# Kernel tuning notes

Hardware: AMD Instinct MI355X
Metric: run time of the kernel (lower is better)

## Reference

```python
import jax, jax.numpy as jnp
import numpy as np

N_NODES = 100000
N_EDGES = 1600000
F_IN, HID, N_CLS = 128, 128, 40


def setup_inputs() -> dict:
    key = jax.random.key(0)
    k1, k2, k3, k4 = jax.random.split(key, 4)
    x = jax.random.normal(k1, (N_NODES, F_IN), dtype=jnp.float32)
    edge_index = jax.random.randint(k2, (2, N_EDGES), 0, N_NODES, dtype=jnp.int64)
    # Glorot-style init for the two GCNConv linear layers
    W1 = jax.random.normal(k3, (F_IN, HID), dtype=jnp.float32) / np.sqrt(F_IN)
    b1 = jnp.zeros((HID,), dtype=jnp.float32)
    W2 = jax.random.normal(k4, (HID, N_CLS), dtype=jnp.float32) / np.sqrt(HID)
    b2 = jnp.zeros((N_CLS,), dtype=jnp.float32)
    return {"x": x, "edge_index": edge_index, "W1": W1, "b1": b1, "W2": W2, "b2": b2}


def gcn_conv(x, src, dst, W, b, n_nodes):
    # x' = D^{-1/2} (A + I) D^{-1/2} X W + b  (PyG GCNConv with default gcn_norm)
    h = x @ W  # [N, out]
    deg = jax.ops.segment_sum(jnp.ones_like(dst, h.dtype), dst, num_segments=n_nodes)
    dinv = jax.lax.rsqrt(deg)  # deg >= 1 because self-loops are included
    norm = dinv[src] * dinv[dst]  # [E']
    msg = h[src] * norm[:, None]  # gather + scale (irregular, memory-bound)
    out = jax.ops.segment_sum(msg, dst, num_segments=n_nodes)  # scatter-add
    return out + b


def reference(x, edge_index, W1, b1, W2, b2):
    n = x.shape[0]
    loops = jnp.arange(n, dtype=edge_index.dtype)
    src = jnp.concatenate([edge_index[0], loops])  # add self-loops once
    dst = jnp.concatenate([edge_index[1], loops])
    h = jax.nn.relu(gcn_conv(x, src, dst, W1, b1, n))
    # dropout is identity in eval mode
    logits = gcn_conv(h, src, dst, W2, b2, n)
    return jax.nn.log_softmax(logits, axis=1)
```

## Files before the change

kernel.cpp:

```cpp
#include <hip/hip_runtime.h>
#include <cstdint>
#include <cmath>

#define F_INN 128
#define HIDD  128
#define NCLS  40

#define BUCK_SHIFT 7
#define BUCK_NODES 128
#define MAXBUCK 1024
#define NSPLIT 8
#define CHUNK 8192

typedef unsigned int u32;
typedef unsigned short u16;
typedef __attribute__((ext_vector_type(8))) short bf16x8;
typedef __attribute__((ext_vector_type(4))) float f32x4;

static __device__ __forceinline__ float bflo(u32 u) { return __builtin_bit_cast(float, u << 16); }
static __device__ __forceinline__ float bfhi(u32 u) { return __builtin_bit_cast(float, u & 0xffff0000u); }
static __device__ __forceinline__ u16 f2bf(float f) {
    u32 u = __builtin_bit_cast(u32, f);
    return (u16)((u + 0x7fffu + ((u >> 16) & 1u)) >> 16);
}
static __device__ __forceinline__ u32 pack2(float a, float b) {
    return (u32)f2bf(a) | ((u32)f2bf(b) << 16);
}


__global__ __launch_bounds__(256) void k_s1(const int* __restrict__ ei, u32* __restrict__ gtot,
                                            int E, int nbuck) {
    __shared__ u32 cnt[MAXBUCK];
    int t = threadIdx.x;
    for (int i = t; i < nbuck; i += 256) cnt[i] = 0;
    __syncthreads();
    int x = blockIdx.x & (NSPLIT - 1);
    int e0 = blockIdx.x * CHUNK;
    int n = min(CHUNK, E - e0);
    const int* dst = ei + E;
    for (int i = t; i < n; i += 256)
        atomicAdd(&cnt[dst[e0 + i] >> BUCK_SHIFT], 1u);
    __syncthreads();
    for (int b = t; b < nbuck; b += 256) {
        u32 c = cnt[b];
        if (c) atomicAdd(&gtot[(b << 3) | x], c);
    }
}


__global__ __launch_bounds__(256) void k_s2(const u32* __restrict__ gtot, u32* __restrict__ base,
                                            u32* __restrict__ cursor, int m) {
    __shared__ u32 part[256];
    int t = threadIdx.x;
    u32 local[32];
    u32 s = 0;
#pragma unroll
    for (int j = 0; j < 32; ++j) {
        int i = t * 32 + j;
        u32 v = (i < m) ? gtot[i] : 0u;
        local[j] = s;
        s += v;
    }
    part[t] = s;
    __syncthreads();
    for (int off = 1; off < 256; off <<= 1) {
        u32 v = (t >= off) ? part[t - off] : 0u;
        __syncthreads();
        part[t] += v;
        __syncthreads();
    }
    u32 pre = (t == 0) ? 0u : part[t - 1];
#pragma unroll
    for (int j = 0; j < 32; ++j) {
        int i = t * 32 + j;
        if (i < m) { u32 bb = pre + local[j]; base[i] = bb; cursor[i] = bb; }
    }
    if (t == 255) base[m] = part[255];
}


__global__ __launch_bounds__(256) void k_s3(const int* __restrict__ ei, u32* __restrict__ cursor,
                                            u32* __restrict__ arr, int E, int nbuck) {
    __shared__ u32 cnt[MAXBUCK];
    __shared__ u32 lbase[MAXBUCK];
    int t = threadIdx.x;
    for (int i = t; i < nbuck; i += 256) cnt[i] = 0;
    __syncthreads();
    int x = blockIdx.x & (NSPLIT - 1);
    int e0 = blockIdx.x * CHUNK;
    int n = min(CHUNK, E - e0);
    const int* src = ei;
    const int* dst = ei + E;
    for (int i = t; i < n; i += 256)
        atomicAdd(&cnt[dst[e0 + i] >> BUCK_SHIFT], 1u);
    __syncthreads();
    for (int b = t; b < nbuck; b += 256) {
        u32 c = cnt[b];
        lbase[b] = c ? atomicAdd(&cursor[(b << 3) | x], c) : 0u;
    }
    __syncthreads();
    for (int i = t; i < nbuck; i += 256) cnt[i] = 0;
    __syncthreads();
    for (int i = t; i < n; i += 256) {
        int s = src[e0 + i], d = dst[e0 + i];
        int b = d >> BUCK_SHIFT;
        u32 off = atomicAdd(&cnt[b], 1u);
        arr[lbase[b] + off] = ((u32)s << BUCK_SHIFT) | (u32)(d & (BUCK_NODES - 1));
    }
}


__global__ __launch_bounds__(256) void k_sortb(const u32* __restrict__ arr, const u32* __restrict__ base,
                                               int* __restrict__ csr, int* __restrict__ rowptr,
                                               float* __restrict__ dinv, int N, int nbuck) {
    __shared__ u32 cnt[BUCK_NODES];
    __shared__ u32 ex[BUCK_NODES];
    __shared__ u32 cur[BUCK_NODES];
    int b = blockIdx.x, t = threadIdx.x;
    int node0 = b << BUCK_SHIFT;
    if (t < BUCK_NODES) cnt[t] = 0;
    __syncthreads();
    u32 s0 = base[b << 3], s1 = base[(b + 1) << 3];
    for (u32 i = s0 + t; i < s1; i += 256)
        atomicAdd(&cnt[arr[i] & (u32)(BUCK_NODES - 1)], 1u);
    __syncthreads();
    if (t < BUCK_NODES) ex[t] = cnt[t];
    __syncthreads();
    for (int off = 1; off < BUCK_NODES; off <<= 1) {
        u32 v = 0;
        if (t < BUCK_NODES && t >= off) v = ex[t - off];
        __syncthreads();
        if (t < BUCK_NODES) ex[t] += v;
        __syncthreads();
    }
    if (t < BUCK_NODES) {
        int node = node0 + t;
        u32 excl = ex[t] - cnt[t];
        cur[t] = s0 + excl;
        if (node <= N) rowptr[node] = (int)(s0 + excl);
        if (node < N) dinv[node] = rsqrtf((float)(cnt[t] + 1));
    }
    if (t == 0 && b == nbuck - 1) rowptr[N] = (int)s1;
    __syncthreads();
    for (u32 i = s0 + t; i < s1; i += 256) {
        u32 pk = arr[i];
        int d = (int)(pk & (u32)(BUCK_NODES - 1));
        u32 pos = atomicAdd(&cur[d], 1u);
        csr[pos] = (int)(pk >> BUCK_SHIFT);
    }
}


__global__ __launch_bounds__(256) void k_gemm1m(const float* __restrict__ X, const float* __restrict__ W,
                                                u32* __restrict__ H, int M) {
    __shared__ u32 xa[128 * 64];
    __shared__ u32 wb[128 * 64];
    int tid = threadIdx.x;
    int row0 = blockIdx.x * 128;
    for (int j = tid; j < 64 * 128; j += 256) {
        int n = j & 127, kp = j >> 7;
        u32 v = pack2(W[(2 * kp) * 128 + n], W[(2 * kp + 1) * 128 + n]);
        wb[n * 64 + (kp ^ ((n & 7) << 2))] = v;
    }
    for (int j = tid; j < 128 * 64; j += 256) {
        int r = j >> 6, c = j & 63;
        int gr = row0 + r;
        u32 v = 0;
        if (gr < M) {
            float2 xv = *(const float2*)&X[(size_t)gr * 128 + 2 * c];
            v = pack2(xv.x, xv.y);
        }
        xa[r * 64 + (c ^ ((r & 7) << 2))] = v;
    }
    __syncthreads();
    int lane = tid & 63, wv = tid >> 6;
    int rw = wv * 32;
    int lr = lane & 15, lg = lane >> 4;
    f32x4 acc[2][8] = {};
    for (int kk = 0; kk < 4; ++kk) {
        int c0 = kk * 16 + lg * 4;
        int ra0 = rw + lr, ra1 = rw + 16 + lr;
        bf16x8 a0 = *(const bf16x8*)&xa[ra0 * 64 + (c0 ^ ((ra0 & 7) << 2))];
        bf16x8 a1 = *(const bf16x8*)&xa[ra1 * 64 + (c0 ^ ((ra1 & 7) << 2))];
#pragma unroll
        for (int nf = 0; nf < 8; ++nf) {
            int bn = nf * 16 + lr;
            bf16x8 bfr = *(const bf16x8*)&wb[bn * 64 + (c0 ^ ((bn & 7) << 2))];
            acc[0][nf] = __builtin_amdgcn_mfma_f32_16x16x32_bf16(a0, bfr, acc[0][nf], 0, 0, 0);
            acc[1][nf] = __builtin_amdgcn_mfma_f32_16x16x32_bf16(a1, bfr, acc[1][nf], 0, 0, 0);
        }
    }
    u16* Hs = (u16*)H;
#pragma unroll
    for (int rf = 0; rf < 2; ++rf) {
#pragma unroll
        for (int nf = 0; nf < 8; ++nf) {
            int col = nf * 16 + lr;
#pragma unroll
            for (int j = 0; j < 4; ++j) {
                int gr = row0 + rw + rf * 16 + lg * 4 + j;
                if (gr < M) Hs[(size_t)gr * 128 + col] = f2bf(acc[rf][nf][j]);
            }
        }
    }
}


__global__ __launch_bounds__(256) void k_gemm2m(const u32* __restrict__ A, const float* __restrict__ W,
                                                u32* __restrict__ H, int M) {
    __shared__ u32 xa[128 * 64];
    __shared__ u32 wb[48 * 64];
    int tid = threadIdx.x;
    int row0 = blockIdx.x * 128;
    for (int j = tid; j < 64 * 64; j += 256) {
        int n = j & 63, kp = j >> 6;
        if (n < 48) {
            u32 v = 0;
            if (n < 40) v = pack2(W[(2 * kp) * 40 + n], W[(2 * kp + 1) * 40 + n]);
            wb[n * 64 + (kp ^ ((n & 7) << 2))] = v;
        }
    }
    for (int j = tid; j < 128 * 64; j += 256) {
        int r = j >> 6, c = j & 63;
        int gr = row0 + r;
        u32 v = (gr < M) ? A[(size_t)gr * 64 + c] : 0u;
        xa[r * 64 + (c ^ ((r & 7) << 2))] = v;
    }
    __syncthreads();
    int lane = tid & 63, wv = tid >> 6;
    int rw = wv * 32;
    int lr = lane & 15, lg = lane >> 4;
    f32x4 acc[2][3] = {};
    for (int kk = 0; kk < 4; ++kk) {
        int c0 = kk * 16 + lg * 4;
        int ra0 = rw + lr, ra1 = rw + 16 + lr;
        bf16x8 a0 = *(const bf16x8*)&xa[ra0 * 64 + (c0 ^ ((ra0 & 7) << 2))];
        bf16x8 a1 = *(const bf16x8*)&xa[ra1 * 64 + (c0 ^ ((ra1 & 7) << 2))];
#pragma unroll
        for (int nf = 0; nf < 3; ++nf) {
            int bn = nf * 16 + lr;
            bf16x8 bfr = *(const bf16x8*)&wb[bn * 64 + (c0 ^ ((bn & 7) << 2))];
            acc[0][nf] = __builtin_amdgcn_mfma_f32_16x16x32_bf16(a0, bfr, acc[0][nf], 0, 0, 0);
            acc[1][nf] = __builtin_amdgcn_mfma_f32_16x16x32_bf16(a1, bfr, acc[1][nf], 0, 0, 0);
        }
    }
    u16* Hs = (u16*)H;
#pragma unroll
    for (int rf = 0; rf < 2; ++rf) {
#pragma unroll
        for (int nf = 0; nf < 3; ++nf) {
            int col = nf * 16 + lr;
            if (col < 40) {
#pragma unroll
                for (int j = 0; j < 4; ++j) {
                    int gr = row0 + rw + rf * 16 + lg * 4 + j;
                    if (gr < M) Hs[(size_t)gr * 64 + col] = f2bf(acc[rf][nf][j]);
                }
            }
        }
    }
}


__global__ __launch_bounds__(256) void k_agg1(const u32* __restrict__ H1, const int* __restrict__ csr,
                                              const int* __restrict__ rowptr, const float* __restrict__ dinv,
                                              const float* __restrict__ b1, u32* __restrict__ A1, int n) {
    int node = (int)((blockIdx.x * 256 + threadIdx.x) >> 6);
    int lane = threadIdx.x & 63;
    if (node >= n) return;
    float di = dinv[node];
    u32 us = H1[(size_t)node * 64 + lane];
    float wself = di * di;
    float ax = wself * bflo(us), ay = wself * bfhi(us);
    int e0 = rowptr[node], e1 = rowptr[node + 1];
    int e = e0;
    for (; e + 3 < e1; e += 4) {
        int s0 = csr[e], s1 = csr[e + 1], s2 = csr[e + 2], s3 = csr[e + 3];
        float w0 = dinv[s0] * di, w1 = dinv[s1] * di, w2 = dinv[s2] * di, w3 = dinv[s3] * di;
        u32 u0 = H1[(size_t)s0 * 64 + lane];
        u32 u1 = H1[(size_t)s1 * 64 + lane];
        u32 u2 = H1[(size_t)s2 * 64 + lane];
        u32 u3 = H1[(size_t)s3 * 64 + lane];
        ax += w0 * bflo(u0) + w1 * bflo(u1) + w2 * bflo(u2) + w3 * bflo(u3);
        ay += w0 * bfhi(u0) + w1 * bfhi(u1) + w2 * bfhi(u2) + w3 * bfhi(u3);
    }
    for (; e < e1; ++e) {
        int s0 = csr[e];
        float w0 = dinv[s0] * di;
        u32 u0 = H1[(size_t)s0 * 64 + lane];
        ax += w0 * bflo(u0);
        ay += w0 * bfhi(u0);
    }
    ax = fmaxf(ax + b1[lane * 2], 0.f);
    ay = fmaxf(ay + b1[lane * 2 + 1], 0.f);
    A1[(size_t)node * 64 + lane] = pack2(ax, ay);
}


__global__ __launch_bounds__(256) void k_agg2(const u32* __restrict__ H2, const int* __restrict__ csr,
                                              const int* __restrict__ rowptr, const float* __restrict__ dinv,
                                              const float* __restrict__ b2, float* __restrict__ out, int n) {
    int wid = (int)((blockIdx.x * 256 + threadIdx.x) >> 6);
    int lane = threadIdx.x & 63;
    int half = lane >> 5, l = lane & 31;
    int node = wid * 2 + half;
    int nc = (node < n) ? node : (n - 1);
    bool wr = (l < 20) && (node < n);
    int idx = (l < 20) ? l : 0;
    float di = dinv[nc];
    u32 us = H2[(size_t)nc * 32 + idx];
    float wself = di * di;
    float a0 = wself * bflo(us), a1 = wself * bfhi(us);
    int e0 = rowptr[nc], e1 = rowptr[nc + 1];
    int e = e0;
    for (; e + 1 < e1; e += 2) {
        int s0 = csr[e], s1 = csr[e + 1];
        float w0 = dinv[s0] * di, w1 = dinv[s1] * di;
        u32 u0 = H2[(size_t)s0 * 32 + idx];
        u32 u1 = H2[(size_t)s1 * 32 + idx];
        a0 += w0 * bflo(u0) + w1 * bflo(u1);
        a1 += w0 * bfhi(u0) + w1 * bfhi(u1);
    }
    if (e < e1) {
        int s0 = csr[e];
        float w0 = dinv[s0] * di;
        u32 u0 = H2[(size_t)s0 * 32 + idx];
        a0 += w0 * bflo(u0);
        a1 += w0 * bfhi(u0);
    }
    a0 += b2[idx * 2];
    a1 += b2[idx * 2 + 1];
    float v = (l < 20) ? fmaxf(a0, a1) : -INFINITY;
#pragma unroll
    for (int off = 16; off > 0; off >>= 1) v = fmaxf(v, __shfl_xor(v, off, 64));
    float ex = (l < 20) ? (expf(a0 - v) + expf(a1 - v)) : 0.f;
#pragma unroll
    for (int off = 16; off > 0; off >>= 1) ex += __shfl_xor(ex, off, 64);
    float ls = logf(ex);
    if (wr) {
        float2 o; o.x = a0 - v - ls; o.y = a1 - v - ls;
        *(float2*)&out[(size_t)node * NCLS + l * 2] = o;
    }
}


extern "C" void kernel_launch(void* const* d_in, const int* in_sizes, int n_in,
                              void* d_out, int out_size, void* d_ws, size_t ws_size,
                              hipStream_t stream) {
    const float* X  = (const float*)d_in[0];
    const int*   EI = (const int*)d_in[1];
    const float* W1 = (const float*)d_in[2];
    const float* B1 = (const float*)d_in[3];
    const float* W2 = (const float*)d_in[4];
    const float* B2 = (const float*)d_in[5];
    float* OUT = (float*)d_out;

    const int N = in_sizes[0] / F_INN;
    const int E = in_sizes[1] / 2;
    const int nbuck = (N + BUCK_NODES - 1) >> BUCK_SHIFT;
    const int m = nbuck * NSPLIT;

    char* ws = (char*)d_ws;
    size_t off = 0;
    auto alloc = [&](size_t bytes) -> void* {
        off = (off + 255) & ~(size_t)255;
        void* p = ws + off;
        off += bytes;
        return p;
    };
    u32*   H1     = (u32*)  alloc((size_t)N * 64 * 4);
    u32*   A1     = (u32*)  alloc((size_t)N * 64 * 4);
    u32*   H2     = (u32*)  alloc((size_t)N * 32 * 4);
    float* dinv   = (float*)alloc((size_t)N * 4);
    u32*   gtot   = (u32*)  alloc((size_t)(m + 1) * 4);
    u32*   base   = (u32*)  alloc((size_t)(m + 1) * 4);
    u32*   cursor = (u32*)  alloc((size_t)m * 4);
    u32*   arr    = (u32*)  alloc((size_t)E * 4);
    int*   csr    = (int*)  alloc((size_t)E * 4);
    int*   rowptr = (int*)  alloc((size_t)(N + 1) * 4);

    hipMemsetAsync(gtot, 0, (size_t)m * 4, stream);

    int nchunk = (E + CHUNK - 1) / CHUNK;

    k_s1   <<<nchunk, 256, 0, stream>>>(EI, gtot, E, nbuck);
    k_s2   <<<1, 256, 0, stream>>>(gtot, base, cursor, m);
    k_s3   <<<nchunk, 256, 0, stream>>>(EI, cursor, arr, E, nbuck);
    k_sortb<<<nbuck, 256, 0, stream>>>(arr, base, csr, rowptr, dinv, N, nbuck);

    int gblk = (N + 127) / 128;
    k_gemm1m<<<gblk, 256, 0, stream>>>(X, W1, H1, N);
    k_agg1  <<<(N + 3) / 4, 256, 0, stream>>>(H1, csr, rowptr, dinv, B1, A1, N);
    k_gemm2m<<<gblk, 256, 0, stream>>>(A1, W2, H2, N);
    int nw = (N + 1) / 2;
    k_agg2  <<<(nw + 3) / 4, 256, 0, stream>>>(H2, csr, rowptr, dinv, B2, OUT, N);
}
```

Measured before the change: 378.5 us.

## Fold source-side degree normalization into GEMM epilogue, drop per-edge dinv gathers

Pre-scales GEMM1 output rows by dinv of the source node, and has agg1 scale its ReLU output by dinv so that GEMM2's output is already source-scaled. Both aggregation kernels then sum raw gathered features and apply the destination dinv once per node, removing the per-edge random dinv[src] loads and multiplies. The aggregation unroll is also widened to 8 and 4 edges to keep more gathers in flight. The pre-scaled values are rounded to bf16 before summation, which slightly changes rounding.

```diff
diff --git a/kernel.cpp b/kernel.cpp
--- a/kernel.cpp
+++ b/kernel.cpp
@@ -152,6 +152,7 @@
 
 
 __global__ __launch_bounds__(256) void k_gemm1m(const float* __restrict__ X, const float* __restrict__ W,
+                                                const float* __restrict__ dinv,
                                                 u32* __restrict__ H, int M) {
     __shared__ u32 xa[128 * 64];
     __shared__ u32 wb[128 * 64];
@@ -190,6 +191,14 @@
             acc[1][nf] = __builtin_amdgcn_mfma_f32_16x16x32_bf16(a1, bfr, acc[1][nf], 0, 0, 0);
         }
     }
+    float drow[2][4];
+#pragma unroll
+    for (int rf = 0; rf < 2; ++rf)
+#pragma unroll
+        for (int j = 0; j < 4; ++j) {
+            int gr = row0 + rw + rf * 16 + lg * 4 + j;
+            drow[rf][j] = (gr < M) ? dinv[gr] : 0.f;
+        }
     u16* Hs = (u16*)H;
 #pragma unroll
     for (int rf = 0; rf < 2; ++rf) {
@@ -199,7 +208,7 @@
 #pragma unroll
             for (int j = 0; j < 4; ++j) {
                 int gr = row0 + rw + rf * 16 + lg * 4 + j;
-                if (gr < M) Hs[(size_t)gr * 128 + col] = f2bf(acc[rf][nf][j]);
+                if (gr < M) Hs[(size_t)gr * 128 + col] = f2bf(acc[rf][nf][j] * drow[rf][j]);
             }
         }
     }
@@ -270,29 +279,34 @@
     if (node >= n) return;
     float di = dinv[node];
     u32 us = H1[(size_t)node * 64 + lane];
-    float wself = di * di;
-    float ax = wself * bflo(us), ay = wself * bfhi(us);
+    float ax = bflo(us), ay = bfhi(us);
     int e0 = rowptr[node], e1 = rowptr[node + 1];
     int e = e0;
-    for (; e + 3 < e1; e += 4) {
+    for (; e + 7 < e1; e += 8) {
         int s0 = csr[e], s1 = csr[e + 1], s2 = csr[e + 2], s3 = csr[e + 3];
-        float w0 = dinv[s0] * di, w1 = dinv[s1] * di, w2 = dinv[s2] * di, w3 = dinv[s3] * di;
+        int s4 = csr[e + 4], s5 = csr[e + 5], s6 = csr[e + 6], s7 = csr[e + 7];
         u32 u0 = H1[(size_t)s0 * 64 + lane];
         u32 u1 = H1[(size_t)s1 * 64 + lane];
         u32 u2 = H1[(size_t)s2 * 64 + lane];
         u32 u3 = H1[(size_t)s3 * 64 + lane];
-        ax += w0 * bflo(u0) + w1 * bflo(u1) + w2 * bflo(u2) + w3 * bflo(u3);
-        ay += w0 * bfhi(u0) + w1 * bfhi(u1) + w2 * bfhi(u2) + w3 * bfhi(u3);
+        u32 u4 = H1[(size_t)s4 * 64 + lane];
+        u32 u5 = H1[(size_t)s5 * 64 + lane];
+        u32 u6 = H1[(size_t)s6 * 64 + lane];
+        u32 u7 = H1[(size_t)s7 * 64 + lane];
+        ax += ((bflo(u0) + bflo(u1)) + (bflo(u2) + bflo(u3)))
+            + ((bflo(u4) + bflo(u5)) + (bflo(u6) + bflo(u7)));
+        ay += ((bfhi(u0) + bfhi(u1)) + (bfhi(u2) + bfhi(u3)))
+            + ((bfhi(u4) + bfhi(u5)) + (bfhi(u6) + bfhi(u7)));
     }
     for (; e < e1; ++e) {
         int s0 = csr[e];
-        float w0 = dinv[s0] * di;
         u32 u0 = H1[(size_t)s0 * 64 + lane];
-        ax += w0 * bflo(u0);
-        ay += w0 * bfhi(u0);
-    }
-    ax = fmaxf(ax + b1[lane * 2], 0.f);
-    ay = fmaxf(ay + b1[lane * 2 + 1], 0.f);
+        ax += bflo(u0);
+        ay += bfhi(u0);
+    }
+    float2 bb = *(const float2*)&b1[lane * 2];
+    ax = fmaxf(di * ax + bb.x, 0.f) * di;
+    ay = fmaxf(di * ay + bb.y, 0.f) * di;
     A1[(size_t)node * 64 + lane] = pack2(ax, ay);
 }
 
@@ -309,27 +323,26 @@
     int idx = (l < 20) ? l : 0;
     float di = dinv[nc];
     u32 us = H2[(size_t)nc * 32 + idx];
-    float wself = di * di;
-    float a0 = wself * bflo(us), a1 = wself * bfhi(us);
+    float a0 = bflo(us), a1 = bfhi(us);
     int e0 = rowptr[nc], e1 = rowptr[nc + 1];
     int e = e0;
-    for (; e + 1 < e1; e += 2) {
-        int s0 = csr[e], s1 = csr[e + 1];
-        float w0 = dinv[s0] * di, w1 = dinv[s1] * di;
+    for (; e + 3 < e1; e += 4) {
+        int s0 = csr[e], s1 = csr[e + 1], s2 = csr[e + 2], s3 = csr[e + 3];
         u32 u0 = H2[(size_t)s0 * 32 + idx];
         u32 u1 = H2[(size_t)s1 * 32 + idx];
-        a0 += w0 * bflo(u0) + w1 * bflo(u1);
-        a1 += w0 * bfhi(u0) + w1 * bfhi(u1);
-    }
-    if (e < e1) {
+        u32 u2 = H2[(size_t)s2 * 32 + idx];
+        u32 u3 = H2[(size_t)s3 * 32 + idx];
+        a0 += (bflo(u0) + bflo(u1)) + (bflo(u2) + bflo(u3));
+        a1 += (bfhi(u0) + bfhi(u1)) + (bfhi(u2) + bfhi(u3));
+    }
+    for (; e < e1; ++e) {
         int s0 = csr[e];
-        float w0 = dinv[s0] * di;
         u32 u0 = H2[(size_t)s0 * 32 + idx];
-        a0 += w0 * bflo(u0);
-        a1 += w0 * bfhi(u0);
-    }
-    a0 += b2[idx * 2];
-    a1 += b2[idx * 2 + 1];
+        a0 += bflo(u0);
+        a1 += bfhi(u0);
+    }
+    a0 = di * a0 + b2[idx * 2];
+    a1 = di * a1 + b2[idx * 2 + 1];
     float v = (l < 20) ? fmaxf(a0, a1) : -INFINITY;
 #pragma unroll
     for (int off = 16; off > 0; off >>= 1) v = fmaxf(v, __shfl_xor(v, off, 64));
@@ -389,7 +402,7 @@
     k_sortb<<<nbuck, 256, 0, stream>>>(arr, base, csr, rowptr, dinv, N, nbuck);
 
     int gblk = (N + 127) / 128;
-    k_gemm1m<<<gblk, 256, 0, stream>>>(X, W1, H1, N);
+    k_gemm1m<<<gblk, 256, 0, stream>>>(X, W1, dinv, H1, N);
     k_agg1  <<<(N + 3) / 4, 256, 0, stream>>>(H1, csr, rowptr, dinv, B1, A1, N);
     k_gemm2m<<<gblk, 256, 0, stream>>>(A1, W2, H2, N);
     int nw = (N + 1) / 2;
```

New measurement: 367.8 us. 2.8% less time.
